# Kernel tuning notes

Hardware: AMD Instinct MI355X
Metric: run time of the kernel (lower is better)

## Reference

```python
import jax, jax.numpy as jnp
import numpy as np

B, T, HID = 2, 2048, 2048
H, KVH, D = 16, 4, 128
N_REP = H // KVH


def _rotate_half(x):
    x1, x2 = jnp.split(x, 2, axis=-1)
    return jnp.concatenate([-x2, x1], axis=-1)


def setup_inputs() -> dict:
    key = jax.random.key(0)
    ks = jax.random.split(key, 8)
    hidden_states = jax.random.normal(ks[0], (B, T, HID), dtype=jnp.float32)
    # RoPE tables: standard theta=10000 frequencies, emb = cat(freqs, freqs)
    inv_freq = 1.0 / (10000.0 ** (np.arange(0, D, 2, dtype=np.float32) / D))
    pos = np.arange(T, dtype=np.float32)
    freqs = np.outer(pos, inv_freq)                      # [T, D/2]
    emb = np.concatenate([freqs, freqs], axis=-1)        # [T, D]
    cos = jnp.broadcast_to(jnp.cos(emb)[None], (B, T, D)).astype(jnp.float32)
    sin = jnp.broadcast_to(jnp.sin(emb)[None], (B, T, D)).astype(jnp.float32)
    # causal additive mask [1,1,T,T]
    neg = jnp.finfo(jnp.float32).min
    causal = jnp.where(jnp.tril(jnp.ones((T, T), dtype=bool)), 0.0, neg)
    attention_mask = causal[None, None].astype(jnp.float32)
    s = 0.02
    Wq = jax.random.normal(ks[1], (H * D, HID), dtype=jnp.float32) * s
    Wk = jax.random.normal(ks[2], (KVH * D, HID), dtype=jnp.float32) * s
    Wv = jax.random.normal(ks[3], (KVH * D, HID), dtype=jnp.float32) * s
    Wo = jax.random.normal(ks[4], (HID, H * D), dtype=jnp.float32) * s
    bq = jnp.zeros((H * D,), dtype=jnp.float32)
    bk = jnp.zeros((KVH * D,), dtype=jnp.float32)
    bv = jnp.zeros((KVH * D,), dtype=jnp.float32)
    return {"hidden_states": hidden_states, "cos": cos, "sin": sin,
            "attention_mask": attention_mask,
            "Wq": Wq, "bq": bq, "Wk": Wk, "bk": bk, "Wv": Wv, "bv": bv, "Wo": Wo}


def reference(hidden_states, cos, sin, attention_mask, Wq, bq, Wk, bk, Wv, bv, Wo):
    bsz, q_len, _ = hidden_states.shape
    q = (jnp.einsum('bth,oh->bto', hidden_states, Wq) + bq).reshape(bsz, q_len, H, D).transpose(0, 2, 1, 3)
    k = (jnp.einsum('bth,oh->bto', hidden_states, Wk) + bk).reshape(bsz, q_len, KVH, D).transpose(0, 2, 1, 3)
    v = (jnp.einsum('bth,oh->bto', hidden_states, Wv) + bv).reshape(bsz, q_len, KVH, D).transpose(0, 2, 1, 3)
    c = cos[:, None, :, :]  # [B,1,T,D]
    s = sin[:, None, :, :]
    q = q * c + _rotate_half(q) * s
    k = k * c + _rotate_half(k) * s
    # repeat KV heads to match Q heads (GQA)
    k = jnp.repeat(k, N_REP, axis=1)  # [B,H,T,D]
    v = jnp.repeat(v, N_REP, axis=1)
    scores = jnp.einsum('bhqd,bhkd->bhqk', q, k) / jnp.sqrt(jnp.float32(D))
    scores = scores + attention_mask
    attn = jax.nn.softmax(scores.astype(jnp.float32), axis=-1).astype(q.dtype)
    out = jnp.einsum('bhqk,bhkd->bhqd', attn, v)          # [B,H,T,D]
    out = out.transpose(0, 2, 1, 3).reshape(bsz, q_len, H * D)
    return jnp.einsum('bto,ho->bth', out, Wo)
```

## Files before the change

### kernel.cpp

```cpp
#include <hip/hip_runtime.h>
#include <hip/hip_bf16.h>
#include <stdint.h>

#define B_ 2
#define T_ 2048
#define HID_ 2048
#define H_ 16
#define KVH_ 4
#define D_ 128

typedef __attribute__((ext_vector_type(8))) short short8;
typedef __attribute__((ext_vector_type(4))) float f32x4;

__device__ __forceinline__ uint16_t f2bf(float x) {
  union { float f; uint32_t u; } c; c.f = x;
  uint32_t r = c.u + 0x7fffu + ((c.u >> 16) & 1u);
  return (uint16_t)(r >> 16);
}
__device__ __forceinline__ float bf2f(uint16_t b) {
  union { uint32_t u; float f; } c; c.u = ((uint32_t)b) << 16;
  return c.f;
}
__device__ __forceinline__ uint16_t hwbf(float x) {
  __hip_bfloat16 h = __float2bfloat16(x);
  return *reinterpret_cast<uint16_t*>(&h);
}

#define XM(r) (((r) & 7) ^ (((r) >> 1) & 4))

__global__ __launch_bounds__(256) void cvt_f32_bf16(const float* __restrict__ in,
                                                    uint16_t* __restrict__ out, int n) {
  int i = (blockIdx.x * 256 + threadIdx.x) * 4;
  if (i >= n) return;
  const float4 v = *reinterpret_cast<const float4*>(in + i);
  union { uint16_t s[4]; uint2 u; } pk;
  pk.s[0] = f2bf(v.x); pk.s[1] = f2bf(v.y); pk.s[2] = f2bf(v.z); pk.s[3] = f2bf(v.w);
  *reinterpret_cast<uint2*>(out + i) = pk.u;
}

__global__ __launch_bounds__(256) void concat_bias(const float* __restrict__ bq,
                                                   const float* __restrict__ bk,
                                                   const float* __restrict__ bv,
                                                   float* __restrict__ out) {
  int i = blockIdx.x * 256 + threadIdx.x;
  if (i < 2048) out[i] = bq[i];
  else if (i < 2560) out[i] = bk[i - 2048];
  else if (i < 3072) out[i] = bv[i - 2560];
}

#define BM 128
#define BN 128
#define BK 64

template<bool OUT_F32, bool HAS_BIAS>
__global__ __launch_bounds__(256, 2) void gemm_bt(const uint16_t* __restrict__ A,
                                                  const uint16_t* __restrict__ Bt,
                                                  void* __restrict__ Cv,
                                                  const float* __restrict__ bias,
                                                  int M, int N, int K) {
  __shared__ __align__(16) uint16_t Al[2][BM * BK];
  __shared__ __align__(16) uint16_t Bl[2][BN * BK];
  const int tid = threadIdx.x;
  const int w = tid >> 6;
  const int lane = tid & 63;
  const int wr = w >> 1, wc = w & 1;
  const int lm = lane & 15, lg = lane >> 4;

  const int GX = gridDim.x;
  const int nwg = GX * gridDim.y;
  int bid = blockIdx.y * GX + blockIdx.x;
  bid = (bid & 7) * (nwg >> 3) + (bid >> 3);
  const int bm = (bid / GX) * BM;
  const int bn = (bid % GX) * BN;

  f32x4 acc[4][4];
  const f32x4 z4 = {0.f, 0.f, 0.f, 0.f};
#pragma unroll
  for (int i = 0; i < 4; ++i)
#pragma unroll
    for (int j = 0; j < 4; ++j) acc[i][j] = z4;

  const int nt = K >> 6;

  auto stage = [&](int b, int t) {
    const int k0 = t * BK;
#pragma unroll
    for (int it = 0; it < 4; ++it) {
      const int chunk = it * 256 + tid;
      const int r = chunk >> 3, c8 = chunk & 7;
      const int csw = (c8 ^ XM(r)) * 8;
      const uint16_t* gA = A + (size_t)(bm + r) * K + k0 + csw;
      const uint16_t* gB = Bt + (size_t)(bn + r) * K + k0 + csw;
      __builtin_amdgcn_global_load_lds((const __attribute__((address_space(1))) unsigned int*)gA,
                                       (__attribute__((address_space(3))) unsigned int*)(&Al[b][0] + chunk * 8),
                                       16, 0, 0);
      __builtin_amdgcn_global_load_lds((const __attribute__((address_space(1))) unsigned int*)gB,
                                       (__attribute__((address_space(3))) unsigned int*)(&Bl[b][0] + chunk * 8),
                                       16, 0, 0);
    }
  };

  stage(0, 0);
  __syncthreads();

  int cur = 0;
  for (int t = 0; t < nt; ++t) {
    if (t + 1 < nt) stage(cur ^ 1, t + 1);
#pragma unroll
    for (int kk = 0; kk < 2; ++kk) {
      short8 af[4], bfr[4];
#pragma unroll
      for (int mi = 0; mi < 4; ++mi) {
        const int r = wr * 64 + mi * 16 + lm;
        af[mi] = *reinterpret_cast<const short8*>(&Al[cur][r * BK + (((kk * 4 + lg) ^ XM(r)) * 8)]);
      }
#pragma unroll
      for (int ni = 0; ni < 4; ++ni) {
        const int r = wc * 64 + ni * 16 + lm;
        bfr[ni] = *reinterpret_cast<const short8*>(&Bl[cur][r * BK + (((kk * 4 + lg) ^ XM(r)) * 8)]);
      }
#pragma unroll
      for (int mi = 0; mi < 4; ++mi)
#pragma unroll
        for (int ni = 0; ni < 4; ++ni)
          acc[mi][ni] = __builtin_amdgcn_mfma_f32_16x16x32_bf16(af[mi], bfr[ni], acc[mi][ni], 0, 0, 0);
    }
    __syncthreads();
    cur ^= 1;
  }

#pragma unroll
  for (int mi = 0; mi < 4; ++mi) {
#pragma unroll
    for (int ni = 0; ni < 4; ++ni) {
      const int col = bn + wc * 64 + ni * 16 + lm;
      float bb = 0.f;
      if (HAS_BIAS) bb = bias[col];
#pragma unroll
      for (int r = 0; r < 4; ++r) {
        const int row = bm + wr * 64 + mi * 16 + lg * 4 + r;
        const float v = acc[mi][ni][r] + bb;
        if (OUT_F32) reinterpret_cast<float*>(Cv)[(size_t)row * N + col] = v;
        else reinterpret_cast<uint16_t*>(Cv)[(size_t)row * N + col] = f2bf(v);
      }
    }
  }
}

#define SC_Q 0.1275523865396698f

__global__ __launch_bounds__(320) void rope_scatter(const uint16_t* __restrict__ raw,
                                                    const float* __restrict__ cosp,
                                                    const float* __restrict__ sinp,
                                                    uint16_t* __restrict__ Qo,
                                                    uint16_t* __restrict__ Ko) {
  const int c8 = threadIdx.x;
  const int m = blockIdx.x;
  const int b = m >> 11, tt = m & 2047;
  const int c = c8 * 8;
  const int d = c & 127;
  const size_t rowoff = (size_t)m * 3072;
  union { short8 v; uint16_t s[8]; } x8, p8, o8;
  x8.v = *reinterpret_cast<const short8*>(raw + rowoff + c);
  p8.v = *reinterpret_cast<const short8*>(raw + rowoff + (c ^ 64));
  const float* cb = cosp + ((size_t)b * T_ + tt) * D_ + d;
  const float* sb = sinp + ((size_t)b * T_ + tt) * D_ + d;
  const bool isq = (c < 2048);
  const float scale = isq ? SC_Q : 1.0f;
  const float sgn = (d < 64) ? -1.f : 1.f;
#pragma unroll
  for (int j = 0; j < 8; ++j) {
    const float x = bf2f(x8.s[j]);
    const float px = bf2f(p8.s[j]);
    o8.s[j] = f2bf((x * cb[j] + sgn * px * sb[j]) * scale);
  }
  if (isq) {
    const int hh = c >> 7;
    *reinterpret_cast<short8*>(Qo + (((size_t)(b * H_ + hh)) * T_ + tt) * D_ + d) = o8.v;
  } else {
    const int hh = (c - 2048) >> 7;
    *reinterpret_cast<short8*>(Ko + (((size_t)(b * KVH_ + hh)) * T_ + tt) * D_ + d) = o8.v;
  }
}

__global__ __launch_bounds__(256) void transpose_v(const uint16_t* __restrict__ raw,
                                                   uint16_t* __restrict__ VtG) {
  const int hb = blockIdx.y;
  const int b = hb >> 2, kvh = hb & 3;
  const int d = threadIdx.x & 127;
  const int tw = threadIdx.x >> 7;
  const int t0 = blockIdx.x * 16 + tw * 8;
  const uint16_t* src = raw + ((size_t)(b * T_ + t0)) * 3072 + 2560 + kvh * 128 + d;
  union { uint16_t s[8]; short8 v; } pk;
#pragma unroll
  for (int j = 0; j < 8; ++j) pk.s[j] = src[(size_t)j * 3072];
  *reinterpret_cast<short8*>(VtG + ((size_t)hb * D_ + d) * T_ + t0) = pk.v;
}

#define KVBLK 64

__global__ __launch_bounds__(256, 4) void attn_fwd(const uint16_t* __restrict__ Qb,
                                                   const uint16_t* __restrict__ Kb,
                                                   const uint16_t* __restrict__ VtG,
                                                   uint16_t* __restrict__ Ab) {
  __shared__ __align__(16) uint16_t Kl[KVBLK * D_];
  __shared__ __align__(16) uint16_t Vtl[D_ * KVBLK];
  __shared__ __align__(16) uint16_t Pl[4 * 16 * 64];
  const int tid = threadIdx.x;
  const int w = tid >> 6, lane = tid & 63;
  const int lm = lane & 15, lg = lane >> 4;
  const int bh = blockIdx.y;
  const int b = bh >> 4, h = bh & 15;
  const int kvh = h >> 2;
  const int qt = (blockIdx.x + bh) & 31;
  const int q0 = qt * 64;
  const int wrow0 = q0 + w * 16;

  const uint16_t* Qw = Qb + (((size_t)(b * H_ + h)) * T_ + wrow0) * D_;
  short8 qf[4];
#pragma unroll
  for (int kk = 0; kk < 4; ++kk)
    qf[kk] = *reinterpret_cast<const short8*>(Qw + (size_t)lm * D_ + kk * 32 + lg * 8);

  f32x4 o[8];
  const f32x4 z4 = {0.f, 0.f, 0.f, 0.f};
#pragma unroll
  for (int f = 0; f < 8; ++f) o[f] = z4;
  f32x4 osum = z4;
  float mrow[4] = {-1e30f, -1e30f, -1e30f, -1e30f};
  short8 vone;
#pragma unroll
  for (int j = 0; j < 8; ++j) vone[j] = (short)0x3F80;

  const uint16_t* Kbase = Kb + ((size_t)(b * KVH_ + kvh)) * T_ * D_;
  const uint16_t* Vtbase = VtG + ((size_t)(b * KVH_ + kvh)) * D_ * T_;
  uint16_t* Pw = Pl + w * 16 * 64;

  const int nkv = qt + 1;
  for (int t = 0; t < nkv; ++t) {
    const int kv0 = t * KVBLK;
    __syncthreads();
#pragma unroll
    for (int it = 0; it < 4; ++it) {
      const int chunk = it * 256 + tid;
      {
        const int r = chunk >> 4, c16 = chunk & 15;
        const uint16_t* g = Kbase + (size_t)(kv0 + r) * D_ + ((c16 ^ XM(r)) * 8);
        __builtin_amdgcn_global_load_lds((const __attribute__((address_space(1))) unsigned int*)g,
                                         (__attribute__((address_space(3))) unsigned int*)(Kl + (it * 256 + w * 64) * 8),
                                         16, 0, 0);
      }
      {
        const int dd = chunk >> 3, c8 = chunk & 7;
        const uint16_t* g = Vtbase + (size_t)dd * T_ + kv0 + ((c8 ^ XM(dd)) * 8);
        __builtin_amdgcn_global_load_lds((const __attribute__((address_space(1))) unsigned int*)g,
                                         (__attribute__((address_space(3))) unsigned int*)(Vtl + (it * 256 + w * 64) * 8),
                                         16, 0, 0);
      }
    }
    __syncthreads();

    f32x4 s[4];
#pragma unroll
    for (int nf = 0; nf < 4; ++nf) s[nf] = z4;
#pragma unroll
    for (int nf = 0; nf < 4; ++nf)
#pragma unroll
      for (int kk = 0; kk < 4; ++kk) {
        const int row = nf * 16 + lm;
        const short8 kf = *reinterpret_cast<const short8*>(Kl + row * D_ + (((kk * 4 + lg) ^ XM(row)) * 8));
        s[nf] = __builtin_amdgcn_mfma_f32_16x16x32_bf16(qf[kk], kf, s[nf], 0, 0, 0);
      }

    if (kv0 + KVBLK - 1 > wrow0) {
#pragma unroll
      for (int nf = 0; nf < 4; ++nf) {
        const int colg = kv0 + nf * 16 + lm;
#pragma unroll
        for (int r = 0; r < 4; ++r) {
          const int rowg = wrow0 + lg * 4 + r;
          if (colg > rowg) s[nf][r] = -1e30f;
        }
      }
    }

    float tmax[4];
#pragma unroll
    for (int r = 0; r < 4; ++r)
      tmax[r] = fmaxf(fmaxf(s[0][r], s[1][r]), fmaxf(s[2][r], s[3][r]));
    bool grow = false;
#pragma unroll
    for (int r = 0; r < 4; ++r) grow = grow || (tmax[r] > mrow[r] + 8.f);
    if (__any((int)grow)) {
#pragma unroll
      for (int r = 0; r < 4; ++r) {
        float v = tmax[r];
        v = fmaxf(v, __shfl_xor(v, 1));
        v = fmaxf(v, __shfl_xor(v, 2));
        v = fmaxf(v, __shfl_xor(v, 4));
        v = fmaxf(v, __shfl_xor(v, 8));
        const float nm = fmaxf(mrow[r], v);
        const float al = exp2f(mrow[r] - nm);
        mrow[r] = nm;
        osum[r] *= al;
#pragma unroll
        for (int f = 0; f < 8; ++f) o[f][r] *= al;
      }
    }
#pragma unroll
    for (int nf = 0; nf < 4; ++nf)
#pragma unroll
      for (int r = 0; r < 4; ++r) {
        const float p = exp2f(s[nf][r] - mrow[r]);
        const int prow = lg * 4 + r;
        const int pchunk = (nf * 2 + (lm >> 3)) ^ XM(prow);
        Pw[prow * 64 + pchunk * 8 + (lm & 7)] = hwbf(p);
      }
    asm volatile("s_waitcnt lgkmcnt(0)" ::: "memory");
    short8 pf[2];
#pragma unroll
    for (int ks = 0; ks < 2; ++ks)
      pf[ks] = *reinterpret_cast<const short8*>(Pw + lm * 64 + (((ks * 4 + lg) ^ XM(lm)) * 8));
#pragma unroll
    for (int ks = 0; ks < 2; ++ks)
      osum = __builtin_amdgcn_mfma_f32_16x16x32_bf16(pf[ks], vone, osum, 0, 0, 0);
#pragma unroll
    for (int f = 0; f < 8; ++f)
#pragma unroll
      for (int ks = 0; ks < 2; ++ks) {
        const int dd = f * 16 + lm;
        const short8 vf = *reinterpret_cast<const short8*>(Vtl + dd * KVBLK + (((ks * 4 + lg) ^ XM(dd)) * 8));
        o[f] = __builtin_amdgcn_mfma_f32_16x16x32_bf16(pf[ks], vf, o[f], 0, 0, 0);
      }
  }

  float rcp[4];
#pragma unroll
  for (int r = 0; r < 4; ++r) rcp[r] = 1.0f / osum[r];
#pragma unroll
  for (int f = 0; f < 8; ++f) {
    const int col = h * D_ + f * 16 + lm;
#pragma unroll
    for (int r = 0; r < 4; ++r) {
      const int trow = wrow0 + lg * 4 + r;
      Ab[((size_t)(b * T_ + trow)) * (H_ * D_) + col] = f2bf(o[f][r] * rcp[r]);
    }
  }
}

extern "C" void kernel_launch(void* const* d_in, const int* in_sizes, int n_in,
                              void* d_out, int out_size, void* d_ws, size_t ws_size,
                              hipStream_t stream) {
  const float* hidden = (const float*)d_in[0];
  const float* cosp   = (const float*)d_in[1];
  const float* sinp   = (const float*)d_in[2];
  const float* Wq = (const float*)d_in[4];
  const float* bq = (const float*)d_in[5];
  const float* Wk = (const float*)d_in[6];
  const float* bk = (const float*)d_in[7];
  const float* Wv = (const float*)d_in[8];
  const float* bv = (const float*)d_in[9];
  const float* Wo = (const float*)d_in[10];

  char* ws = (char*)d_ws;
  uint16_t* hidb   = (uint16_t*)(ws);
  uint16_t* wqkv   = (uint16_t*)(ws + 16777216);
  uint16_t* wob    = (uint16_t*)(ws + 29360128);
  float*    biasq  = (float*)   (ws + 37748736);
  uint16_t* qkvraw = (uint16_t*)(ws + 37761024);
  uint16_t* Qb     = (uint16_t*)(ws + 62926848);
  uint16_t* Kb     = (uint16_t*)(ws + 79704064);
  uint16_t* VtG    = (uint16_t*)(ws + 83898368);
  uint16_t* Ab     = (uint16_t*)(ws + 88092672);

  cvt_f32_bf16<<<8192, 256, 0, stream>>>(hidden, hidb, 8388608);
  cvt_f32_bf16<<<4096, 256, 0, stream>>>(Wq, wqkv, 4194304);
  cvt_f32_bf16<<<1024, 256, 0, stream>>>(Wk, wqkv + 4194304, 1048576);
  cvt_f32_bf16<<<1024, 256, 0, stream>>>(Wv, wqkv + 5242880, 1048576);
  cvt_f32_bf16<<<4096, 256, 0, stream>>>(Wo, wob, 4194304);
  concat_bias<<<12, 256, 0, stream>>>(bq, bk, bv, biasq);

  gemm_bt<false, true><<<dim3(24, 32), 256, 0, stream>>>(hidb, wqkv, qkvraw, biasq, 4096, 3072, 2048);
  rope_scatter<<<4096, 320, 0, stream>>>(qkvraw, cosp, sinp, Qb, Kb);
  transpose_v<<<dim3(128, 8), 256, 0, stream>>>(qkvraw, VtG);
  attn_fwd<<<dim3(32, 32), 256, 0, stream>>>(Qb, Kb, VtG, Ab);
  gemm_bt<true, false><<<dim3(16, 32), 256, 0, stream>>>(Ab, wob, d_out, nullptr, 4096, 2048, 2048);
}
```

Baseline: 241.1 us.

## Pair causal query tiles per block and double-buffer K/V staging in attention

Each attention block now processes two query tiles, qt and 31-qt, so every block does the same 33 KV iterations and the causal load imbalance goes away. The grid is halved to match. K and V tiles are double-buffered in LDS, with the next tile's async global-to-LDS load issued before the current tile's compute, overlapping memory with MFMA work. This doubles LDS use and lowers the launch_bounds occupancy hint from 4 to 2 blocks, which could reduce latency hiding.

New measurement: 228.0 us. 5.4% less time.

```diff
diff --git a/kernel.cpp b/kernel.cpp
--- a/kernel.cpp
+++ b/kernel.cpp
@@ -199,12 +199,12 @@
 
 #define KVBLK 64
 
-__global__ __launch_bounds__(256, 4) void attn_fwd(const uint16_t* __restrict__ Qb,
+__global__ __launch_bounds__(256, 2) void attn_fwd(const uint16_t* __restrict__ Qb,
                                                    const uint16_t* __restrict__ Kb,
                                                    const uint16_t* __restrict__ VtG,
                                                    uint16_t* __restrict__ Ab) {
-  __shared__ __align__(16) uint16_t Kl[KVBLK * D_];
-  __shared__ __align__(16) uint16_t Vtl[D_ * KVBLK];
+  __shared__ __align__(16) uint16_t Kl[2][KVBLK * D_];
+  __shared__ __align__(16) uint16_t Vtl[2][D_ * KVBLK];
   __shared__ __align__(16) uint16_t Pl[4 * 16 * 64];
   const int tid = threadIdx.x;
   const int w = tid >> 6, lane = tid & 63;
@@ -212,34 +212,54 @@
   const int bh = blockIdx.y;
   const int b = bh >> 4, h = bh & 15;
   const int kvh = h >> 2;
-  const int qt = (blockIdx.x + bh) & 31;
-  const int q0 = qt * 64;
-  const int wrow0 = q0 + w * 16;
-
-  const uint16_t* Qw = Qb + (((size_t)(b * H_ + h)) * T_ + wrow0) * D_;
-  short8 qf[4];
-#pragma unroll
-  for (int kk = 0; kk < 4; ++kk)
-    qf[kk] = *reinterpret_cast<const short8*>(Qw + (size_t)lm * D_ + kk * 32 + lg * 8);
-
-  f32x4 o[8];
-  const f32x4 z4 = {0.f, 0.f, 0.f, 0.f};
-#pragma unroll
-  for (int f = 0; f < 8; ++f) o[f] = z4;
-  f32x4 osum = z4;
-  float mrow[4] = {-1e30f, -1e30f, -1e30f, -1e30f};
-  short8 vone;
-#pragma unroll
-  for (int j = 0; j < 8; ++j) vone[j] = (short)0x3F80;
+  const int qtA = (blockIdx.x + bh) & 15;
+  const int qtB = 31 - qtA;
+  const int nA = qtA + 1;
+  const int ntot = 33;
 
   const uint16_t* Kbase = Kb + ((size_t)(b * KVH_ + kvh)) * T_ * D_;
   const uint16_t* Vtbase = VtG + ((size_t)(b * KVH_ + kvh)) * D_ * T_;
   uint16_t* Pw = Pl + w * 16 * 64;
-
-  const int nkv = qt + 1;
-  for (int t = 0; t < nkv; ++t) {
-    const int kv0 = t * KVBLK;
-    __syncthreads();
+  const f32x4 z4 = {0.f, 0.f, 0.f, 0.f};
+
+  short8 vone;
+#pragma unroll
+  for (int j = 0; j < 8; ++j) vone[j] = (short)0x3F80;
+
+  f32x4 o[8];
+  f32x4 osum;
+  float mrow[4];
+  short8 qf[4];
+
+  auto loadQ = [&](int qt) {
+    const uint16_t* Qw = Qb + (((size_t)(b * H_ + h)) * T_ + qt * 64 + w * 16) * D_;
+#pragma unroll
+    for (int kk = 0; kk < 4; ++kk)
+      qf[kk] = *reinterpret_cast<const short8*>(Qw + (size_t)lm * D_ + kk * 32 + lg * 8);
+  };
+  auto resetAcc = [&]() {
+#pragma unroll
+    for (int f = 0; f < 8; ++f) o[f] = z4;
+    osum = z4;
+#pragma unroll
+    for (int r = 0; r < 4; ++r) mrow[r] = -1e30f;
+  };
+  auto flush = [&](int qt) {
+    const int wr0 = qt * 64 + w * 16;
+    float rcp[4];
+#pragma unroll
+    for (int r = 0; r < 4; ++r) rcp[r] = 1.0f / osum[r];
+#pragma unroll
+    for (int f = 0; f < 8; ++f) {
+      const int col = h * D_ + f * 16 + lm;
+#pragma unroll
+      for (int r = 0; r < 4; ++r) {
+        const int trow = wr0 + lg * 4 + r;
+        Ab[((size_t)(b * T_ + trow)) * (H_ * D_) + col] = f2bf(o[f][r] * rcp[r]);
+      }
+    }
+  };
+  auto stage = [&](int buf, int kv0) {
 #pragma unroll
     for (int it = 0; it < 4; ++it) {
       const int chunk = it * 256 + tid;
@@ -247,18 +267,37 @@
         const int r = chunk >> 4, c16 = chunk & 15;
         const uint16_t* g = Kbase + (size_t)(kv0 + r) * D_ + ((c16 ^ XM(r)) * 8);
         __builtin_amdgcn_global_load_lds((const __attribute__((address_space(1))) unsigned int*)g,
-                                         (__attribute__((address_space(3))) unsigned int*)(Kl + (it * 256 + w * 64) * 8),
+                                         (__attribute__((address_space(3))) unsigned int*)(&Kl[buf][0] + (it * 256 + w * 64) * 8),
                                          16, 0, 0);
       }
       {
         const int dd = chunk >> 3, c8 = chunk & 7;
         const uint16_t* g = Vtbase + (size_t)dd * T_ + kv0 + ((c8 ^ XM(dd)) * 8);
         __builtin_amdgcn_global_load_lds((const __attribute__((address_space(1))) unsigned int*)g,
-                                         (__attribute__((address_space(3))) unsigned int*)(Vtl + (it * 256 + w * 64) * 8),
+                                         (__attribute__((address_space(3))) unsigned int*)(&Vtl[buf][0] + (it * 256 + w * 64) * 8),
                                          16, 0, 0);
       }
     }
-    __syncthreads();
+  };
+
+  loadQ(qtA);
+  resetAcc();
+  stage(0, 0);
+  __syncthreads();
+
+  int cur = 0;
+  for (int g = 0; g < ntot; ++g) {
+    const bool inA = g < nA;
+    const int t = inA ? g : g - nA;
+    const int qt = inA ? qtA : qtB;
+    const int kv0 = t * KVBLK;
+    const int wrow0 = qt * 64 + w * 16;
+
+    if (g + 1 < ntot) {
+      const int gn = g + 1;
+      const int kvn = (gn < nA ? gn : gn - nA) * KVBLK;
+      stage(cur ^ 1, kvn);
+    }
 
     f32x4 s[4];
 #pragma unroll
@@ -268,7 +307,7 @@
 #pragma unroll
       for (int kk = 0; kk < 4; ++kk) {
         const int row = nf * 16 + lm;
-        const short8 kf = *reinterpret_cast<const short8*>(Kl + row * D_ + (((kk * 4 + lg) ^ XM(row)) * 8));
+        const short8 kf = *reinterpret_cast<const short8*>(&Kl[cur][row * D_ + (((kk * 4 + lg) ^ XM(row)) * 8)]);
         s[nf] = __builtin_amdgcn_mfma_f32_16x16x32_bf16(qf[kk], kf, s[nf], 0, 0, 0);
       }
 
@@ -329,23 +368,20 @@
 #pragma unroll
       for (int ks = 0; ks < 2; ++ks) {
         const int dd = f * 16 + lm;
-        const short8 vf = *reinterpret_cast<const short8*>(Vtl + dd * KVBLK + (((ks * 4 + lg) ^ XM(dd)) * 8));
+        const short8 vf = *reinterpret_cast<const short8*>(&Vtl[cur][dd * KVBLK + (((ks * 4 + lg) ^ XM(dd)) * 8)]);
         o[f] = __builtin_amdgcn_mfma_f32_16x16x32_bf16(pf[ks], vf, o[f], 0, 0, 0);
       }
+
+    __syncthreads();
+    cur ^= 1;
+
+    if (g == nA - 1) {
+      flush(qtA);
+      loadQ(qtB);
+      resetAcc();
+    }
   }
-
-  float rcp[4];
-#pragma unroll
-  for (int r = 0; r < 4; ++r) rcp[r] = 1.0f / osum[r];
-#pragma unroll
-  for (int f = 0; f < 8; ++f) {
-    const int col = h * D_ + f * 16 + lm;
-#pragma unroll
-    for (int r = 0; r < 4; ++r) {
-      const int trow = wrow0 + lg * 4 + r;
-      Ab[((size_t)(b * T_ + trow)) * (H_ * D_) + col] = f2bf(o[f][r] * rcp[r]);
-    }
-  }
+  flush(qtB);
 }
 
 extern "C" void kernel_launch(void* const* d_in, const int* in_sizes, int n_in,
@@ -383,6 +419,6 @@
   gemm_bt<false, true><<<dim3(24, 32), 256, 0, stream>>>(hidb, wqkv, qkvraw, biasq, 4096, 3072, 2048);
   rope_scatter<<<4096, 320, 0, stream>>>(qkvraw, cosp, sinp, Qb, Kb);
   transpose_v<<<dim3(128, 8), 256, 0, stream>>>(qkvraw, VtG);
-  attn_fwd<<<dim3(32, 32), 256, 0, stream>>>(Qb, Kb, VtG, Ab);
+  attn_fwd<<<dim3(16, 32), 256, 0, stream>>>(Qb, Kb, VtG, Ab);
   gemm_bt<true, false><<<dim3(16, 32), 256, 0, stream>>>(Ab, wob, d_out, nullptr, 4096, 2048, 2048);
 }
```
